# Optimization experiments

Hardware: AMD Instinct MI355X
Metric: run time of the kernel (lower is better)

The kernel has to match this reference:

```python
import jax, jax.numpy as jnp
import numpy as np

D_MODEL = 512
N_HEADS = 8


def setup_inputs() -> dict:
    key = jax.random.key(0)
    ks = jax.random.split(key, 16)
    bs, S, D = 16, 512, D_MODEL
    def lin(k, fo, fi):
        lim = np.sqrt(6.0 / (fi + fo)).astype(np.float32)
        return jax.random.uniform(k, (fo, fi), jnp.float32, -lim, lim)
    inp = {
        'q': jax.random.normal(ks[0], (bs, S, D), jnp.float32),
        'k': jax.random.normal(ks[1], (bs, S, D), jnp.float32),
        'v': jax.random.normal(ks[2], (bs, S, D), jnp.float32),
        'sgap': jax.random.randint(ks[3], (bs, S), 0, 100, jnp.int64) if jax.config.jax_enable_x64 else jax.random.randint(ks[3], (bs, S), 0, 100, jnp.int32),
        'pcount': jax.random.randint(ks[4], (bs, S), 0, 50, jnp.int32),
        'Wq': lin(ks[5], D, D), 'bq': jnp.zeros((D,), jnp.float32),
        'Wk': lin(ks[6], D, D), 'bk': jnp.zeros((D,), jnp.float32),
        'Wv': lin(ks[7], D, D), 'bv': jnp.zeros((D,), jnp.float32),
        'Wo': lin(ks[8], D, D), 'bo': jnp.zeros((D,), jnp.float32),
        'gammas': jax.random.normal(ks[9], (N_HEADS, 1, 1), jnp.float32) * 0.5,
        'ln_g': jnp.ones((D,), jnp.float32), 'ln_b': jnp.zeros((D,), jnp.float32),
        'Wi1': lin(ks[10], D // 4, 2), 'bi1': jnp.zeros((D // 4,), jnp.float32),
        'Wi2': lin(ks[11], D, D // 4), 'bi2': jnp.zeros((D,), jnp.float32),
        'iscale': jnp.array([0.5], jnp.float32),
    }
    return inp


def reference(q, k, v, sgap, pcount, Wq, bq, Wk, bk, Wv, bv, Wo, bo, gammas, ln_g, ln_b, Wi1, bi1, Wi2, bi2, iscale):
    bs, S, D = q.shape
    h = gammas.shape[0]
    d_k = D // h
    def split_heads(x, W, b):
        return (x @ W.T + b).reshape(bs, S, h, d_k).transpose(0, 2, 1, 3)  # [b,h,S,d]
    qh = split_heads(q, Wq, bq)
    kh = split_heads(k, Wk, bk)
    vh = split_heads(v, Wv, bv)

    scores = jnp.einsum('bhid,bhjd->bhij', qh, kh) / jnp.sqrt(jnp.float32(d_k))
    # strict-causal mask (triu(ones,k=0)==0): attend only to j < i
    mask = jnp.tril(jnp.ones((S, S), bool), k=-1)[None, None]
    NEG = jnp.float32(-1e32)

    # no-grad temporal distance term
    p = jax.nn.softmax(jnp.where(mask, scores, NEG), axis=-1) * mask
    distcum = jnp.cumsum(p, axis=-1)
    disttotal = jnp.sum(p, axis=-1, keepdims=True)
    idx = jnp.arange(S, dtype=jnp.float32)
    pos = jnp.abs(idx[None, :] - idx[:, None])[None, None]
    dist = jax.lax.stop_gradient(jnp.sqrt(jnp.clip((disttotal - distcum) * pos, 0.0, None)))

    gam = -jax.nn.softplus(gammas)[None]  # [1,h,1,1]
    temporal = jnp.clip(jnp.exp(dist * gam), 1e-5, 1e5)
    attn = jax.nn.softmax(jnp.where(mask, scores * temporal, NEG), axis=-1)
    attn = attn.at[:, :, 0, :].set(0.0)  # zero_pad first query position

    X = jnp.einsum('bhij,bhjd->bhid', attn, vh).transpose(0, 2, 1, 3).reshape(bs, S, D)

    # InterferenceAddNorm
    def norm01(x):
        x = x.astype(jnp.float32)
        std = jnp.std(x, ddof=1) + 1e-6
        return (jnp.tanh((x - jnp.mean(x)) / std) + 1.0) / 2.0
    ii = jnp.stack([norm01(sgap), norm01(pcount)], axis=-1)  # [b,S,2]
    feat = jax.nn.relu(ii @ Wi1.T + bi1) @ Wi2.T + bi2
    Y = X + iscale * feat
    mu = jnp.mean(Y, -1, keepdims=True)
    var = jnp.var(Y, -1, keepdims=True)
    Yn = (Y - mu) / jnp.sqrt(var + 1e-5) * ln_g + ln_b
    return Yn @ Wo.T + bo
```

## Files before the change

### kernel.cpp

```cpp
#include <hip/hip_runtime.h>
#include <hip/hip_bf16.h>
#include <math.h>

typedef __attribute__((ext_vector_type(8))) short bf16x8;
typedef __attribute__((ext_vector_type(4))) float f32x4;
typedef __fp16 __attribute__((ext_vector_type(2))) h16x2;

__device__ __forceinline__ f32x4 mfma16(bf16x8 a, bf16x8 b, f32x4 c) {
  return __builtin_amdgcn_mfma_f32_16x16x32_bf16(a, b, c, 0, 0, 0);
}

__device__ __forceinline__ float scan16(float x) {
  int v;
  v = __builtin_amdgcn_update_dpp(0, __float_as_int(x), 0x111, 0xf, 0xf, true);
  x += __int_as_float(v);
  v = __builtin_amdgcn_update_dpp(0, __float_as_int(x), 0x112, 0xf, 0xf, true);
  x += __int_as_float(v);
  v = __builtin_amdgcn_update_dpp(0, __float_as_int(x), 0x114, 0xf, 0xf, true);
  x += __int_as_float(v);
  v = __builtin_amdgcn_update_dpp(0, __float_as_int(x), 0x118, 0xf, 0xf, true);
  x += __int_as_float(v);
  return x;
}

__global__ void stats_kernel(const int* __restrict__ sgap,
                             const int* __restrict__ pcount,
                             float* __restrict__ stats) {
  const int N = 16 * 512;
  long long s0 = 0, q0 = 0, s1 = 0, q1 = 0;
  for (int i = threadIdx.x; i < N; i += 256) {
    long long a = sgap[i];
    long long b = pcount[i];
    s0 += a; q0 += a * a;
    s1 += b; q1 += b * b;
  }
#pragma unroll
  for (int m = 32; m >= 1; m >>= 1) {
    s0 += __shfl_xor(s0, m, 64); q0 += __shfl_xor(q0, m, 64);
    s1 += __shfl_xor(s1, m, 64); q1 += __shfl_xor(q1, m, 64);
  }
  __shared__ long long red[4][4];
  const int w = threadIdx.x >> 6;
  if ((threadIdx.x & 63) == 0) {
    red[w][0] = s0; red[w][1] = q0; red[w][2] = s1; red[w][3] = q1;
  }
  __syncthreads();
  if (threadIdx.x == 0) {
    long long S0 = 0, Q0 = 0, S1 = 0, Q1 = 0;
    for (int i = 0; i < 4; ++i) {
      S0 += red[i][0]; Q0 += red[i][1]; S1 += red[i][2]; Q1 += red[i][3];
    }
    const double n = (double)N;
    const double mean0 = S0 / n, mean1 = S1 / n;
    const double var0 = ((double)Q0 - (double)S0 * (double)S0 / n) / (n - 1.0);
    const double var1 = ((double)Q1 - (double)S1 * (double)S1 / n) / (n - 1.0);
    const float std0 = (float)sqrt(var0) + 1e-6f;
    const float std1 = (float)sqrt(var1) + 1e-6f;
    stats[0] = (float)mean0; stats[1] = 1.0f / std0;
    stats[2] = (float)mean1; stats[3] = 1.0f / std1;
  }
}

__global__ __launch_bounds__(256) void cvtW_kernel(
    const float* __restrict__ Wq, const float* __restrict__ Wk,
    const float* __restrict__ Wv, const float* __restrict__ Wo,
    __hip_bfloat16* __restrict__ Wbf) {
  const int i = blockIdx.x * 256 + threadIdx.x;
  const int sel = i >> 16;
  const int off = i & 65535;
  const float* W = (sel == 0) ? Wq : (sel == 1) ? Wk : (sel == 2) ? Wv : Wo;
  const float4 x = *(const float4*)(W + (size_t)off * 4);
  union { __hip_bfloat16 h[4]; uint2 u; } ub;
  ub.h[0] = __float2bfloat16(x.x); ub.h[1] = __float2bfloat16(x.y);
  ub.h[2] = __float2bfloat16(x.z); ub.h[3] = __float2bfloat16(x.w);
  *(uint2*)(Wbf + (size_t)i * 4) = ub.u;
}

template <int AMODE>
__device__ __forceinline__ void gemm_body(const void* __restrict__ Ain,
                                          const __hip_bfloat16* __restrict__ Wb,
                                          const float* __restrict__ bias,
                                          void* __restrict__ Out, const int omode,
                                          const int tm, const int tn) {
  constexpr int LDK = 40;
  __shared__ __hip_bfloat16 As[128 * LDK];
  __shared__ __hip_bfloat16 Bs[128 * LDK];
  const int tid = threadIdx.x;
  const int lane = tid & 63;
  const int wid = tid >> 6;
  const int wm = (wid >> 1) * 64;
  const int wn = (wid & 1) * 64;
  const int g = lane >> 4, l15 = lane & 15;

  const f32x4 Z = {0.f, 0.f, 0.f, 0.f};
  f32x4 acc[4][4];
#pragma unroll
  for (int m = 0; m < 4; ++m)
#pragma unroll
    for (int n = 0; n < 4; ++n) acc[m][n] = Z;

  for (int k0 = 0; k0 < 512; k0 += 32) {
#pragma unroll
    for (int p = 0; p < 4; ++p) {
      const int c = p * 256 + tid;
      const int row = c >> 3;
      const int kc = (c & 7) * 4;
      union { __hip_bfloat16 h[4]; uint2 u; } ua;
      if (AMODE == 0) {
        const float4 x = *(const float4*)((const float*)Ain + (size_t)(tm + row) * 512 + k0 + kc);
        ua.h[0] = __float2bfloat16(x.x); ua.h[1] = __float2bfloat16(x.y);
        ua.h[2] = __float2bfloat16(x.z); ua.h[3] = __float2bfloat16(x.w);
      } else {
        ua.u = *(const uint2*)((const __hip_bfloat16*)Ain + (size_t)(tm + row) * 512 + k0 + kc);
      }
      *(uint2*)&As[row * LDK + kc] = ua.u;
    }
#pragma unroll
    for (int p = 0; p < 2; ++p) {
      const int c = p * 256 + tid;
      const int row = c >> 2;
      const int kc = (c & 3) * 8;
      *(uint4*)&Bs[row * LDK + kc] =
          *(const uint4*)(Wb + (size_t)(tn + row) * 512 + k0 + kc);
    }
    __syncthreads();
    bf16x8 af[4], bfv[4];
#pragma unroll
    for (int m = 0; m < 4; ++m)
      af[m] = *(const bf16x8*)&As[(wm + m * 16 + l15) * LDK + g * 8];
#pragma unroll
    for (int n = 0; n < 4; ++n)
      bfv[n] = *(const bf16x8*)&Bs[(wn + n * 16 + l15) * LDK + g * 8];
#pragma unroll
    for (int m = 0; m < 4; ++m)
#pragma unroll
      for (int n = 0; n < 4; ++n)
        acc[m][n] = mfma16(af[m], bfv[n], acc[m][n]);
    __syncthreads();
  }

#pragma unroll
  for (int n = 0; n < 4; ++n) {
    const int cc = tn + wn + n * 16 + l15;
    const float bv = bias[cc];
#pragma unroll
    for (int m = 0; m < 4; ++m) {
#pragma unroll
      for (int jj = 0; jj < 4; ++jj) {
        const int r = tm + wm + m * 16 + g * 4 + jj;
        const float v = acc[m][n][jj] + bv;
        if (omode == 2) {
          ((float*)Out)[(size_t)r * 512 + cc] = v;
        } else {
          const int bb = r >> 9, srow = r & 511, hh = cc >> 6, dd = cc & 63;
          if (omode == 0)
            ((__hip_bfloat16*)Out)[(((size_t)(bb * 8 + hh)) * 512 + srow) * 64 + dd] =
                __float2bfloat16(v);
          else
            ((__hip_bfloat16*)Out)[(((size_t)(bb * 8 + hh)) * 64 + dd) * 512 + srow] =
                __float2bfloat16(v);
        }
      }
    }
  }
}

__global__ __launch_bounds__(256) void gemm_qkv(
    const float* __restrict__ q, const float* __restrict__ k,
    const float* __restrict__ v, const float* __restrict__ bq,
    const float* __restrict__ bk, const float* __restrict__ bv,
    const __hip_bfloat16* __restrict__ Wbf, __hip_bfloat16* __restrict__ qh,
    __hip_bfloat16* __restrict__ kh, __hip_bfloat16* __restrict__ vhT) {
  const int flat = blockIdx.x + 4 * blockIdx.y + 256 * blockIdx.z;
  const int L = (flat & 7) * 96 + (flat >> 3);
  const int z = L >> 8;
  const int rem = L & 255;
  const int tm = (rem >> 2) * 128;
  const int tn = (rem & 3) * 128;
  const float* A = (z == 0) ? q : (z == 1) ? k : v;
  const float* bias = (z == 0) ? bq : (z == 1) ? bk : bv;
  void* Out = (z == 0) ? (void*)qh : (z == 1) ? (void*)kh : (void*)vhT;
  gemm_body<0>(A, Wbf + (size_t)z * (512 * 512), bias, Out, (z == 2) ? 1 : 0, tm, tn);
}

__global__ __launch_bounds__(256) void gemm_wo(const __hip_bfloat16* __restrict__ Yn,
                                               const __hip_bfloat16* __restrict__ Wbf,
                                               const float* __restrict__ bo,
                                               float* __restrict__ Out) {
  const int flat = blockIdx.x + 4 * blockIdx.y;
  const int L = (flat & 7) * 32 + (flat >> 3);
  const int tm = (L >> 2) * 128;
  const int tn = (L & 3) * 128;
  gemm_body<1>(Yn, Wbf + (size_t)3 * (512 * 512), bo, Out, 2, tm, tn);
}

#define PLD 40

__device__ __forceinline__ void attn_unit(
    const __hip_bfloat16* __restrict__ Q, const __hip_bfloat16* __restrict__ K,
    const __hip_bfloat16* __restrict__ V, __hip_bfloat16* __restrict__ Xb,
    __hip_bfloat16* Pw, const int i0, const int ntile, const float gam,
    const int b, const int h, const int lane) {
  const int g = lane >> 4, l15 = lane & 15;
  const float scale = 0.125f;
  const f32x4 Z = {0.f, 0.f, 0.f, 0.f};

  const bf16x8 qf0 = *(const bf16x8*)&Q[(i0 + l15) * 64 + g * 8];
  const bf16x8 qf1 = *(const bf16x8*)&Q[(i0 + l15) * 64 + 32 + g * 8];

  h16x2 sp[64];
  float d1p[4] = {0.f, 0.f, 0.f, 0.f};
#pragma unroll
  for (int t = 0; t < 32; ++t) {
    if (t < ntile) {
      const bf16x8 kf0 = *(const bf16x8*)&K[(t * 16 + l15) * 64 + g * 8];
      const bf16x8 kf1 = *(const bf16x8*)&K[(t * 16 + l15) * 64 + 32 + g * 8];
      f32x4 s = mfma16(qf0, kf0, Z);
      s = mfma16(qf1, kf1, s);
      sp[2 * t] = __builtin_amdgcn_cvt_pkrtz(s[0] * scale, s[1] * scale);
      sp[2 * t + 1] = __builtin_amdgcn_cvt_pkrtz(s[2] * scale, s[3] * scale);
      const int j = t * 16 + l15;
#pragma unroll
      for (int jj = 0; jj < 4; ++jj) {
        const float sv = (float)((jj < 2) ? sp[2 * t][jj] : sp[2 * t + 1][jj - 2]);
        const int i = i0 + g * 4 + jj;
        d1p[jj] += (j < i) ? __expf(sv) : 0.f;
      }
    }
  }
  float invd1[4];
#pragma unroll
  for (int jj = 0; jj < 4; ++jj) {
    float dd = d1p[jj];
#pragma unroll
    for (int m = 8; m >= 1; m >>= 1) dd += __shfl_xor(dd, m, 16);
    invd1[jj] = dd > 0.f ? 1.f / dd : 0.f;
  }

  f32x4 accx[4] = {Z, Z, Z, Z};
  float carry[4] = {0.f, 0.f, 0.f, 0.f};
  float d2p[4] = {0.f, 0.f, 0.f, 0.f};

#pragma unroll
  for (int tp = 0; tp < 16; ++tp) {
    if (tp * 2 < ntile) {
      __hip_bfloat16* Pb = Pw + (tp & 1) * (16 * PLD);
#pragma unroll
      for (int half = 0; half < 2; ++half) {
        const int t = tp * 2 + half;
        float e2v[4] = {0.f, 0.f, 0.f, 0.f};
        if (t < ntile) {
          const int j = t * 16 + l15;
#pragma unroll
          for (int jj = 0; jj < 4; ++jj) {
            const float sv = (float)((jj < 2) ? sp[2 * t][jj] : sp[2 * t + 1][jj - 2]);
            const int i = i0 + g * 4 + jj;
            const bool valid = j < i;
            const float p = valid ? __expf(sv) * invd1[jj] : 0.f;
            const float cs = scan16(p) + carry[jj];
            const float suffix = 1.f - cs;
            carry[jj] = __shfl(cs, 15, 16);
            const float dist = sqrtf(fmaxf(suffix * (float)(i - j), 0.f));
            const float tempo = fmaxf(__expf(gam * dist), 1e-5f);
            const float e2 = valid ? __expf(sv * tempo) : 0.f;
            d2p[jj] += e2;
            e2v[jj] = e2;
          }
        }
#pragma unroll
        for (int jj = 0; jj < 4; ++jj)
          Pb[(g * 4 + jj) * PLD + half * 16 + l15] = __float2bfloat16(e2v[jj]);
      }
      asm volatile("s_waitcnt lgkmcnt(0)" ::: "memory");
      const bf16x8 pf = *(const bf16x8*)&Pb[l15 * PLD + g * 8];
#pragma unroll
      for (int n = 0; n < 4; ++n) {
        const bf16x8 vf =
            *(const bf16x8*)&V[(size_t)(n * 16 + l15) * 512 + tp * 32 + g * 8];
        accx[n] = mfma16(pf, vf, accx[n]);
      }
    }
  }

#pragma unroll
  for (int jj = 0; jj < 4; ++jj) {
    float dd = d2p[jj];
#pragma unroll
    for (int m = 8; m >= 1; m >>= 1) dd += __shfl_xor(dd, m, 16);
    d2p[jj] = dd > 0.f ? 1.f / dd : 0.f;
  }
#pragma unroll
  for (int n = 0; n < 4; ++n) {
#pragma unroll
    for (int jj = 0; jj < 4; ++jj) {
      const int i = i0 + g * 4 + jj;
      const float val = (i > 0) ? accx[n][jj] * d2p[jj] : 0.f;
      Xb[((size_t)(b * 512 + i)) * 512 + h * 64 + n * 16 + l15] = __float2bfloat16(val);
    }
  }
}

__global__ __launch_bounds__(64) void attn_kernel(
    const __hip_bfloat16* __restrict__ qh, const __hip_bfloat16* __restrict__ kh,
    const __hip_bfloat16* __restrict__ vhT, const float* __restrict__ gammas,
    __hip_bfloat16* __restrict__ Xb) {
  __shared__ __hip_bfloat16 Psh[2 * 16 * PLD];
  const int lane = threadIdx.x;
  const int work = (blockIdx.x & 7) * 512 + (blockIdx.x >> 3);
  const int bh = work >> 5;
  const int rg = work & 31;
  const int b = bh >> 3, h = bh & 7;

  const __hip_bfloat16* Q = qh + (size_t)bh * (512 * 64);
  const __hip_bfloat16* K = kh + (size_t)bh * (512 * 64);
  const __hip_bfloat16* V = vhT + (size_t)bh * (64 * 512);
  const float gam = -log1pf(expf(gammas[h]));

  attn_unit(Q, K, V, Xb, Psh, rg * 16, rg + 1, gam, b, h, lane);
}

__global__ __launch_bounds__(256) void addnorm_kernel(
    const __hip_bfloat16* __restrict__ Xb, const int* __restrict__ sgap,
    const int* __restrict__ pcount, const float* __restrict__ stats,
    const float* __restrict__ Wi1, const float* __restrict__ bi1,
    const float* __restrict__ Wi2, const float* __restrict__ bi2,
    const float* __restrict__ iscale, const float* __restrict__ ln_g,
    const float* __restrict__ ln_b, __hip_bfloat16* __restrict__ Yn) {
  constexpr int WLD = 132;
  __shared__ __hip_bfloat16 Hs[16 * WLD];
  __shared__ float iis[16][2];
  __shared__ float red[4][16][2];
  const int tid = threadIdx.x;
  const int lane = tid & 63;
  const int w = tid >> 6;
  const int g = lane >> 4, l15 = lane & 15;
  const int t0 = blockIdx.x * 16;

  if (tid < 16) {
    const float a0 = ((float)sgap[t0 + tid] - stats[0]) * stats[1];
    const float a1 = ((float)pcount[t0 + tid] - stats[2]) * stats[3];
    iis[tid][0] = (tanhf(a0) + 1.f) * 0.5f;
    iis[tid][1] = (tanhf(a1) + 1.f) * 0.5f;
  }
  __syncthreads();

  {
    const int tt = tid & 15;
    const int jb = (tid >> 4) * 8;
    const float a = iis[tt][0], b = iis[tt][1];
#pragma unroll
    for (int jj = 0; jj < 8; ++jj) {
      const int j = jb + jj;
      const float hv = fmaxf(Wi1[j * 2] * a + Wi1[j * 2 + 1] * b + bi1[j], 0.f);
      Hs[tt * WLD + j] = __float2bfloat16(hv);
    }
  }
  __syncthreads();

  const f32x4 Z = {0.f, 0.f, 0.f, 0.f};
  f32x4 acc[8];
#pragma unroll
  for (int n = 0; n < 8; ++n) acc[n] = Z;

#pragma unroll
  for (int k = 0; k < 4; ++k) {
    const bf16x8 af = *(const bf16x8*)&Hs[l15 * WLD + k * 32 + g * 8];
#pragma unroll
    for (int n = 0; n < 8; ++n) {
      const int col = w * 128 + n * 16 + l15;
      const float4 x0 = *(const float4*)(Wi2 + (size_t)col * 128 + k * 32 + g * 8);
      const float4 x1 = *(const float4*)(Wi2 + (size_t)col * 128 + k * 32 + g * 8 + 4);
      union { __hip_bfloat16 hh[8]; bf16x8 v8; } ub;
      ub.hh[0] = __float2bfloat16(x0.x); ub.hh[1] = __float2bfloat16(x0.y);
      ub.hh[2] = __float2bfloat16(x0.z); ub.hh[3] = __float2bfloat16(x0.w);
      ub.hh[4] = __float2bfloat16(x1.x); ub.hh[5] = __float2bfloat16(x1.y);
      ub.hh[6] = __float2bfloat16(x1.z); ub.hh[7] = __float2bfloat16(x1.w);
      acc[n] = mfma16(af, ub.v8, acc[n]);
    }
  }

  const float sc = iscale[0];
  float bi[8], lg[8], lb[8];
#pragma unroll
  for (int nn = 0; nn < 8; ++nn) {
    const int c = w * 128 + nn * 16 + l15;
    bi[nn] = bi2[c]; lg[nn] = ln_g[c]; lb[nn] = ln_b[c];
  }

#pragma unroll
  for (int jj = 0; jj < 4; ++jj) {
    const int r = g * 4 + jj;
    float s = 0.f, sq = 0.f;
#pragma unroll
    for (int nn = 0; nn < 8; ++nn) {
      const int c = w * 128 + nn * 16 + l15;
      const float fv = acc[nn][jj] + bi[nn];
      const float y = __bfloat162float(Xb[(size_t)(t0 + r) * 512 + c]) + sc * fv;
      acc[nn][jj] = y;
      s += y; sq += y * y;
    }
#pragma unroll
    for (int mk = 8; mk >= 1; mk >>= 1) {
      s += __shfl_xor(s, mk, 16);
      sq += __shfl_xor(sq, mk, 16);
    }
    if (l15 == 0) { red[w][r][0] = s; red[w][r][1] = sq; }
  }
  __syncthreads();

#pragma unroll
  for (int jj = 0; jj < 4; ++jj) {
    const int r = g * 4 + jj;
    const float sum = red[0][r][0] + red[1][r][0] + red[2][r][0] + red[3][r][0];
    const float sqs = red[0][r][1] + red[1][r][1] + red[2][r][1] + red[3][r][1];
    const float mu = sum * (1.f / 512.f);
    const float var = sqs * (1.f / 512.f) - mu * mu;
    const float rstd = rsqrtf(var + 1e-5f);
#pragma unroll
    for (int nn = 0; nn < 8; ++nn) {
      const int c = w * 128 + nn * 16 + l15;
      Yn[(size_t)(t0 + r) * 512 + c] =
          __float2bfloat16((acc[nn][jj] - mu) * rstd * lg[nn] + lb[nn]);
    }
  }
}

extern "C" void kernel_launch(void* const* d_in, const int* in_sizes, int n_in,
                              void* d_out, int out_size, void* d_ws, size_t ws_size,
                              hipStream_t stream) {
  const float* q = (const float*)d_in[0];
  const float* k = (const float*)d_in[1];
  const float* v = (const float*)d_in[2];
  const int* sgap = (const int*)d_in[3];
  const int* pcount = (const int*)d_in[4];
  const float* Wq = (const float*)d_in[5];
  const float* bq = (const float*)d_in[6];
  const float* Wk = (const float*)d_in[7];
  const float* bk = (const float*)d_in[8];
  const float* Wv = (const float*)d_in[9];
  const float* bv = (const float*)d_in[10];
  const float* Wo = (const float*)d_in[11];
  const float* bo = (const float*)d_in[12];
  const float* gammas = (const float*)d_in[13];
  const float* ln_g = (const float*)d_in[14];
  const float* ln_b = (const float*)d_in[15];
  const float* Wi1 = (const float*)d_in[16];
  const float* bi1 = (const float*)d_in[17];
  const float* Wi2 = (const float*)d_in[18];
  const float* bi2 = (const float*)d_in[19];
  const float* iscale = (const float*)d_in[20];

  char* ws = (char*)d_ws;
  __hip_bfloat16* qh = (__hip_bfloat16*)(ws);
  __hip_bfloat16* kh = (__hip_bfloat16*)(ws + ((size_t)8 << 20));
  __hip_bfloat16* vhT = (__hip_bfloat16*)(ws + ((size_t)16 << 20));
  __hip_bfloat16* Xb = (__hip_bfloat16*)(ws + ((size_t)24 << 20));
  __hip_bfloat16* Yn = (__hip_bfloat16*)(ws + ((size_t)32 << 20));
  __hip_bfloat16* Wbf = (__hip_bfloat16*)(ws + ((size_t)40 << 20));
  float* stats = (float*)(ws + ((size_t)42 << 20));

  stats_kernel<<<1, 256, 0, stream>>>(sgap, pcount, stats);
  cvtW_kernel<<<1024, 256, 0, stream>>>(Wq, Wk, Wv, Wo, Wbf);
  gemm_qkv<<<dim3(4, 64, 3), 256, 0, stream>>>(q, k, v, bq, bk, bv, Wbf,
                                               qh, kh, vhT);
  attn_kernel<<<4096, 64, 0, stream>>>(qh, kh, vhT, gammas, Xb);
  addnorm_kernel<<<512, 256, 0, stream>>>(Xb, sgap, pcount, stats, Wi1, bi1, Wi2,
                                          bi2, iscale, ln_g, ln_b, Yn);
  gemm_wo<<<dim3(4, 64), 256, 0, stream>>>(Yn, Wbf, bo, (float*)d_out);
}
```

Measured before the change: 279.6 us.

## Prefetch GEMM tiles into registers with BK=64 and pair causal attention rows

```diff
diff --git a/kernel.cpp b/kernel.cpp
--- a/kernel.cpp
+++ b/kernel.cpp
@@ -82,7 +82,7 @@
                                           const float* __restrict__ bias,
                                           void* __restrict__ Out, const int omode,
                                           const int tm, const int tn) {
-  constexpr int LDK = 40;
+  constexpr int LDK = 72;
   __shared__ __hip_bfloat16 As[128 * LDK];
   __shared__ __hip_bfloat16 Bs[128 * LDK];
   const int tid = threadIdx.x;
@@ -99,43 +99,66 @@
 #pragma unroll
     for (int n = 0; n < 4; ++n) acc[m][n] = Z;
 
-  for (int k0 = 0; k0 < 512; k0 += 32) {
+  float4 pa[8];
+  uint2 pa16[8];
+  uint4 pb[4];
+
+  auto LOAD = [&](int k0) {
+#pragma unroll
+    for (int p = 0; p < 8; ++p) {
+      const int c = p * 256 + tid;
+      const int row = c >> 4, kc = (c & 15) * 4;
+      if (AMODE == 0)
+        pa[p] = *(const float4*)((const float*)Ain + (size_t)(tm + row) * 512 + k0 + kc);
+      else
+        pa16[p] = *(const uint2*)((const __hip_bfloat16*)Ain + (size_t)(tm + row) * 512 + k0 + kc);
+    }
 #pragma unroll
     for (int p = 0; p < 4; ++p) {
       const int c = p * 256 + tid;
-      const int row = c >> 3;
-      const int kc = (c & 7) * 4;
+      const int row = c >> 3, kc = (c & 7) * 8;
+      pb[p] = *(const uint4*)(Wb + (size_t)(tn + row) * 512 + k0 + kc);
+    }
+  };
+
+  LOAD(0);
+  for (int k0 = 0; k0 < 512; k0 += 64) {
+#pragma unroll
+    for (int p = 0; p < 8; ++p) {
+      const int c = p * 256 + tid;
+      const int row = c >> 4, kc = (c & 15) * 4;
       union { __hip_bfloat16 h[4]; uint2 u; } ua;
       if (AMODE == 0) {
-        const float4 x = *(const float4*)((const float*)Ain + (size_t)(tm + row) * 512 + k0 + kc);
-        ua.h[0] = __float2bfloat16(x.x); ua.h[1] = __float2bfloat16(x.y);
-        ua.h[2] = __float2bfloat16(x.z); ua.h[3] = __float2bfloat16(x.w);
+        ua.h[0] = __float2bfloat16(pa[p].x); ua.h[1] = __float2bfloat16(pa[p].y);
+        ua.h[2] = __float2bfloat16(pa[p].z); ua.h[3] = __float2bfloat16(pa[p].w);
       } else {
-        ua.u = *(const uint2*)((const __hip_bfloat16*)Ain + (size_t)(tm + row) * 512 + k0 + kc);
+        ua.u = pa16[p];
       }
       *(uint2*)&As[row * LDK + kc] = ua.u;
     }
 #pragma unroll
-    for (int p = 0; p < 2; ++p) {
+    for (int p = 0; p < 4; ++p) {
       const int c = p * 256 + tid;
-      const int row = c >> 2;
-      const int kc = (c & 3) * 8;
-      *(uint4*)&Bs[row * LDK + kc] =
-          *(const uint4*)(Wb + (size_t)(tn + row) * 512 + k0 + kc);
+      const int row = c >> 3, kc = (c & 7) * 8;
+      *(uint4*)&Bs[row * LDK + kc] = pb[p];
     }
     __syncthreads();
-    bf16x8 af[4], bfv[4];
-#pragma unroll
-    for (int m = 0; m < 4; ++m)
-      af[m] = *(const bf16x8*)&As[(wm + m * 16 + l15) * LDK + g * 8];
-#pragma unroll
-    for (int n = 0; n < 4; ++n)
-      bfv[n] = *(const bf16x8*)&Bs[(wn + n * 16 + l15) * LDK + g * 8];
-#pragma unroll
-    for (int m = 0; m < 4; ++m)
+    if (k0 + 64 < 512) LOAD(k0 + 64);
+#pragma unroll
+    for (int kk = 0; kk < 2; ++kk) {
+      bf16x8 af[4], bfv[4];
+#pragma unroll
+      for (int m = 0; m < 4; ++m)
+        af[m] = *(const bf16x8*)&As[(wm + m * 16 + l15) * LDK + kk * 32 + g * 8];
 #pragma unroll
       for (int n = 0; n < 4; ++n)
-        acc[m][n] = mfma16(af[m], bfv[n], acc[m][n]);
+        bfv[n] = *(const bf16x8*)&Bs[(wn + n * 16 + l15) * LDK + kk * 32 + g * 8];
+#pragma unroll
+      for (int m = 0; m < 4; ++m)
+#pragma unroll
+        for (int n = 0; n < 4; ++n)
+          acc[m][n] = mfma16(af[m], bfv[n], acc[m][n]);
+    }
     __syncthreads();
   }
 
@@ -306,9 +329,9 @@
     __hip_bfloat16* __restrict__ Xb) {
   __shared__ __hip_bfloat16 Psh[2 * 16 * PLD];
   const int lane = threadIdx.x;
-  const int work = (blockIdx.x & 7) * 512 + (blockIdx.x >> 3);
-  const int bh = work >> 5;
-  const int rg = work & 31;
+  const int work = (blockIdx.x & 7) * 256 + (blockIdx.x >> 3);
+  const int bh = work >> 4;
+  const int pr = work & 15;
   const int b = bh >> 3, h = bh & 7;
 
   const __hip_bfloat16* Q = qh + (size_t)bh * (512 * 64);
@@ -316,7 +339,8 @@
   const __hip_bfloat16* V = vhT + (size_t)bh * (64 * 512);
   const float gam = -log1pf(expf(gammas[h]));
 
-  attn_unit(Q, K, V, Xb, Psh, rg * 16, rg + 1, gam, b, h, lane);
+  attn_unit(Q, K, V, Xb, Psh, pr * 16, pr + 1, gam, b, h, lane);
+  attn_unit(Q, K, V, Xb, Psh, (31 - pr) * 16, 32 - pr, gam, b, h, lane);
 }
 
 __global__ __launch_bounds__(256) void addnorm_kernel(
@@ -463,7 +487,7 @@
   cvtW_kernel<<<1024, 256, 0, stream>>>(Wq, Wk, Wv, Wo, Wbf);
   gemm_qkv<<<dim3(4, 64, 3), 256, 0, stream>>>(q, k, v, bq, bk, bv, Wbf,
                                                qh, kh, vhT);
-  attn_kernel<<<4096, 64, 0, stream>>>(qh, kh, vhT, gammas, Xb);
+  attn_kernel<<<2048, 64, 0, stream>>>(qh, kh, vhT, gammas, Xb);
   addnorm_kernel<<<512, 256, 0, stream>>>(Xb, sgap, pcount, stats, Wi1, bi1, Wi2,
                                           bi2, iscale, ln_g, ln_b, Yn);
   gemm_wo<<<dim3(4, 64), 256, 0, stream>>>(Yn, Wbf, bo, (float*)d_out);
```

Result: slower. 346.4 us (+23.9%).
